# Optimization experiments

Measured on AMD Instinct MI355X. Metric: run time of the kernel, lower is better.

The kernel has to match this reference:

```python
import jax, jax.numpy as jnp
import numpy as np

B, S, D, H = 4, 2048, 512, 8

def setup_inputs() -> dict:
    key = jax.random.key(0)
    ks = jax.random.split(key, 6)
    query = jax.random.normal(ks[0], (B, S, D), dtype=jnp.float32)
    value = jax.random.normal(ks[1], (B, S, D), dtype=jnp.float32)
    # causal additive mask, broadcast over heads: [H, S, S]
    causal = jnp.where(jnp.tril(jnp.ones((S, S), dtype=bool)), 0.0, -1e9).astype(jnp.float32)
    mask = jnp.broadcast_to(causal[None, :, :], (H, S, S))
    sd = 1.0 / np.sqrt(D)
    Wq = jax.random.normal(ks[2], (D, D), dtype=jnp.float32) * sd
    Wkv = jax.random.normal(ks[3], (D, 2 * D), dtype=jnp.float32) * sd
    Wo = jax.random.normal(ks[4], (D, D), dtype=jnp.float32) * sd
    normalizer = jnp.asarray(1.0 / np.sqrt(D // H), dtype=jnp.float32)  # 1/sqrt(head_size)
    head_mults = jnp.ones((1, 1, H, 1), dtype=jnp.float32)
    return {"query": query, "value": value, "mask": mask, "Wq": Wq, "Wkv": Wkv,
            "Wo": Wo, "normalizer": normalizer, "head_mults": head_mults}

def reference(query, value, mask, Wq, Wkv, Wo, normalizer, head_mults):
    b, sq, d = query.shape
    h = head_mults.shape[2]
    q = (query @ Wq).reshape(b, sq, h, -1)                 # [b,q,h,hd]
    k, v = jnp.split(value @ Wkv, 2, axis=-1)
    sk = value.shape[1]
    k = k.reshape(b, sk, h, -1)
    v = v.reshape(b, sk, h, -1)
    score = jnp.einsum('bqhd,bkhd->bhqk', q, k) * normalizer
    score = score + mask[None, :, :, :]
    align = jax.nn.softmax(score, axis=-1)
    heads = jnp.einsum('bhqk,bkhd->bqhd', align, v)        # [b,q,h,hd]
    # cross-head normalization (over head axis, ddof=0 like tf.reduce_std)
    mean = jnp.mean(heads, axis=-2, keepdims=True)
    std = jnp.std(heads, axis=-2, keepdims=True)
    heads = (heads - mean) / (std + 0.01)
    heads = heads * head_mults
    out = heads.reshape(b, sq, d) @ Wo
    return out
```

## Files before the change

### kernel.cpp

```cpp
#include <hip/hip_runtime.h>


typedef float  f32x4  __attribute__((ext_vector_type(4)));
typedef __bf16 bf16x8 __attribute__((ext_vector_type(8)));
typedef short  s16x4  __attribute__((ext_vector_type(4)));
typedef unsigned short u16;

#define BS 2048
#define DD 512
#define NH 8
#define NQ (4 * BS * DD)

__device__ __forceinline__ u16 f2bf(float f) {
  union { float f; unsigned u; } v; v.f = f;
  unsigned r = v.u + 0x7fffu + ((v.u >> 16) & 1u);
  return (u16)(r >> 16);
}
__device__ __forceinline__ float bf2f(u16 b) {
  union { unsigned u; float f; } v; v.u = ((unsigned)b) << 16; return v.f;
}

__device__ __forceinline__ void gll16(const u16* g, u16* l) {
  __builtin_amdgcn_global_load_lds((const __attribute__((address_space(1))) void*)g,
                                   (__attribute__((address_space(3))) void*)l, 16, 0, 0);
}

__global__ __launch_bounds__(256) void prep(const float* __restrict__ q,
                                            const float* __restrict__ v,
                                            const float* __restrict__ Wq,
                                            const float* __restrict__ Wkv,
                                            const float* __restrict__ Wo,
                                            u16* __restrict__ qb, u16* __restrict__ vb,
                                            u16* __restrict__ WqT, u16* __restrict__ WkvT,
                                            u16* __restrict__ WoT) {
  __shared__ float Ts[64][65];
  const int t = threadIdx.x;
  int bx = blockIdx.x;
  if (bx < 8192) {
    int i = (bx * 256 + t) * 4;
    const float* s; u16* d;
    if (i < NQ) { s = q + i; d = qb + i; }
    else        { s = v + (i - NQ); d = vb + (i - NQ); }
    float4 x = *(const float4*)s;
    ushort4 o; o.x = f2bf(x.x); o.y = f2bf(x.y); o.z = f2bf(x.z); o.w = f2bf(x.w);
    *(ushort4*)d = o;
    return;
  }
  int tb = bx - 8192;
  const float* W; u16* Wt; int N, ntn;
  if (tb < 64)       { W = Wq;  Wt = WqT;  N = 512;  ntn = 8; }
  else if (tb < 192) { W = Wkv; Wt = WkvT; N = 1024; ntn = 16; tb -= 64; }
  else               { W = Wo;  Wt = WoT;  N = 512;  ntn = 8;  tb -= 192; }
  int tk = tb / ntn, tn = tb - tk * ntn;
  int r = t >> 2, c0 = (t & 3) * 16;
  const float* src = &W[(long)(tk * 64 + r) * N + tn * 64 + c0];
#pragma unroll
  for (int j = 0; j < 4; ++j) {
    float4 x = *(const float4*)(src + j * 4);
    Ts[r][c0 + j * 4 + 0] = x.x; Ts[r][c0 + j * 4 + 1] = x.y;
    Ts[r][c0 + j * 4 + 2] = x.z; Ts[r][c0 + j * 4 + 3] = x.w;
  }
  __syncthreads();
  u16* dst = &Wt[(long)(tn * 64 + r) * 512 + tk * 64 + c0];
#pragma unroll
  for (int m = 0; m < 4; ++m) {
    ushort4 o;
    o.x = f2bf(Ts[c0 + m * 4 + 0][r]); o.y = f2bf(Ts[c0 + m * 4 + 1][r]);
    o.z = f2bf(Ts[c0 + m * 4 + 2][r]); o.w = f2bf(Ts[c0 + m * 4 + 3][r]);
    *(ushort4*)(dst + m * 4) = o;
  }
}

__device__ __forceinline__ void gemm_core(const u16* __restrict__ A,
                                          const u16* __restrict__ Bt,
                                          int m0, int n0, int K,
                                          u16* Al, u16* Bl, f32x4 acc[4][4]) {
  const int t = threadIdx.x;
  const int wv = t >> 6, ln = t & 63, qd = ln >> 4, l16 = ln & 15;
  const int rw = (wv & 1) * 64, cw = (wv >> 1) * 64;
  const int sr = wv * 16 + (ln >> 2), sc = (ln & 3) * 8;
  for (int k0 = 0; k0 < K; k0 += 32) {
    __syncthreads();
#pragma unroll
    for (int c = 0; c < 2; ++c) {
      int r = c * 64 + sr;
      gll16(&A[(long)(m0 + r) * K + k0 + sc], &Al[r * 32 + sc]);
      gll16(&Bt[(long)(n0 + r) * K + k0 + sc], &Bl[r * 32 + sc]);
    }
    __syncthreads();
    bf16x8 af[4], bfr[4];
#pragma unroll
    for (int i = 0; i < 4; ++i) af[i] = *(const bf16x8*)&Al[(rw + i * 16 + l16) * 32 + qd * 8];
#pragma unroll
    for (int j = 0; j < 4; ++j) bfr[j] = *(const bf16x8*)&Bl[(cw + j * 16 + l16) * 32 + qd * 8];
#pragma unroll
    for (int i = 0; i < 4; ++i)
#pragma unroll
      for (int j = 0; j < 4; ++j)
        acc[i][j] = __builtin_amdgcn_mfma_f32_16x16x32_bf16(af[i], bfr[j], acc[i][j], 0, 0, 0);
  }
}

__global__ __launch_bounds__(256) void qkv_gemm(const u16* __restrict__ qA,
                                                const u16* __restrict__ vA,
                                                const u16* __restrict__ WqT,
                                                const u16* __restrict__ WkvT,
                                                u16* __restrict__ Qb,
                                                u16* __restrict__ Kb,
                                                u16* __restrict__ Vt) {
  __shared__ __align__(16) u16 Al[128 * 32];
  __shared__ __align__(16) u16 Bl[128 * 32];
  const bool isQ = blockIdx.y < 4;
  const u16* A = isQ ? qA : vA;
  const u16* Bt = isQ ? WqT : WkvT;
  const int n0 = (isQ ? blockIdx.y : blockIdx.y - 4) * 128;
  const int m0 = blockIdx.x * 128;
  f32x4 acc[4][4] = {};
  gemm_core(A, Bt, m0, n0, 512, Al, Bl, acc);
  const int t = threadIdx.x;
  const int wv = t >> 6, ln = t & 63, qd = ln >> 4, l16 = ln & 15;
  const int rw = (wv & 1) * 64, cw = (wv >> 1) * 64;
  if (isQ) {
#pragma unroll
    for (int i = 0; i < 4; ++i)
#pragma unroll
      for (int j = 0; j < 4; ++j) {
        int row = m0 + rw + i * 16 + qd * 4, col = n0 + cw + j * 16 + l16;
#pragma unroll
        for (int r = 0; r < 4; ++r)
          Qb[(long)(row + r) * 512 + col] = f2bf(acc[i][j][r]);
      }
  } else {
#pragma unroll
    for (int j = 0; j < 4; ++j) {
      int col = n0 + cw + j * 16 + l16;
      if (col < 512) {
#pragma unroll
        for (int i = 0; i < 4; ++i) {
          int row = m0 + rw + i * 16 + qd * 4;
#pragma unroll
          for (int r = 0; r < 4; ++r)
            Kb[(long)(row + r) * 512 + col] = f2bf(acc[i][j][r]);
        }
      } else {
        int c2 = col - 512, hh = c2 >> 6, dd = c2 & 63;
#pragma unroll
        for (int i = 0; i < 4; ++i) {
          int sg = m0 + rw + i * 16 + qd * 4;
          int bb = sg >> 11, ss = sg & 2047;
          ushort4 o;
          o.x = f2bf(acc[i][j][0]); o.y = f2bf(acc[i][j][1]);
          o.z = f2bf(acc[i][j][2]); o.w = f2bf(acc[i][j][3]);
          *(ushort4*)&Vt[((long)(bb * 8 + hh) * 64 + dd) * 2048 + ss] = o;
        }
      }
    }
  }
}

__global__ __launch_bounds__(256) void out_gemm(const u16* __restrict__ A,
                                                const u16* __restrict__ Bt,
                                                float* __restrict__ C) {
  __shared__ __align__(16) u16 Al[128 * 32];
  __shared__ __align__(16) u16 Bl[128 * 32];
  const int m0 = blockIdx.x * 128, n0 = blockIdx.y * 128;
  f32x4 acc[4][4] = {};
  gemm_core(A, Bt, m0, n0, 512, Al, Bl, acc);
  const int t = threadIdx.x;
  const int wv = t >> 6, ln = t & 63, qd = ln >> 4, l16 = ln & 15;
  const int rw = (wv & 1) * 64, cw = (wv >> 1) * 64;
#pragma unroll
  for (int i = 0; i < 4; ++i)
#pragma unroll
    for (int j = 0; j < 4; ++j) {
      int row = m0 + rw + i * 16 + qd * 4, col = n0 + cw + j * 16 + l16;
#pragma unroll
      for (int r = 0; r < 4; ++r)
        C[(long)(row + r) * 512 + col] = acc[i][j][r];
    }
}

__global__ __launch_bounds__(256, 4) void attn(const u16* __restrict__ Qb,
                                               const u16* __restrict__ Kb,
                                               const u16* __restrict__ Vt,
                                               u16* __restrict__ heads,
                                               const float* __restrict__ normp) {
  constexpr int ST = 72;
  __shared__ __align__(16) u16 Ks[2][64 * ST];
  __shared__ __align__(16) u16 Vts[2][64 * ST];
  const float scale2 = normp[0] * 1.44269504f;
  const int t = threadIdx.x;
  const int wv = t >> 6, ln = t & 63, qd = ln >> 4, l16 = ln & 15;
  const int sr = t >> 2, scg = (t & 3) * 16;
  const int h = blockIdx.y, b = blockIdx.z;
  const int bs0 = b * BS;
  const u16* vtb = Vt + ((long)(b * 8 + h) * 64) * 2048;

  for (int qsel = 0; qsel < 2; ++qsel) {
    const int qt = qsel ? (31 - (int)blockIdx.x) : (int)blockIdx.x;
    const int qi = qt * 64 + wv * 16 + l16;

    bf16x8 bq[2];
#pragma unroll
    for (int c = 0; c < 2; ++c)
      bq[c] = *(const bf16x8*)&Qb[(long)(bs0 + qi) * 512 + h * 64 + c * 32 + qd * 8];

    bf16x8 kr0, kr1, vr0, vr1;
#define FETCH(KB) do { \
      const u16* kp_ = &Kb[(long)(bs0 + (KB) * 64 + sr) * 512 + h * 64 + scg]; \
      kr0 = *(const bf16x8*)kp_; kr1 = *(const bf16x8*)(kp_ + 8); \
      const u16* vp_ = &vtb[(long)sr * 2048 + (KB) * 64 + scg]; \
      vr0 = *(const bf16x8*)vp_; vr1 = *(const bf16x8*)(vp_ + 8); } while (0)
    FETCH(0);
    float m_i = -1e30f, l_i = 0.f;
    f32x4 o[4] = {};

    for (int kb = 0; kb <= qt; ++kb) {
      const int buf = kb & 1;
      *(bf16x8*)&Ks[buf][sr * ST + scg] = kr0;
      *(bf16x8*)&Ks[buf][sr * ST + scg + 8] = kr1;
      *(bf16x8*)&Vts[buf][sr * ST + scg] = vr0;
      *(bf16x8*)&Vts[buf][sr * ST + scg + 8] = vr1;
      __syncthreads();
      if (kb < qt) FETCH(kb + 1);

      f32x4 s[4] = {};
#pragma unroll
      for (int c = 0; c < 2; ++c)
#pragma unroll
        for (int nt = 0; nt < 4; ++nt) {
          bf16x8 ak = *(const bf16x8*)&Ks[buf][(nt * 16 + l16) * ST + c * 32 + qd * 8];
          s[nt] = __builtin_amdgcn_mfma_f32_16x16x32_bf16(ak, bq[c], s[nt], 0, 0, 0);
        }

      const int limi = (kb == qt) ? (wv * 16 + l16) : 1 << 20;
      float mx = -1e30f;
#pragma unroll
      for (int nt = 0; nt < 4; ++nt)
#pragma unroll
        for (int r = 0; r < 4; ++r) {
          float v = s[nt][r] * scale2;
          if (nt * 16 + qd * 4 + r > limi) v = -1e30f;
          s[nt][r] = v;
          mx = fmaxf(mx, v);
        }
      mx = fmaxf(mx, __shfl_xor(mx, 16));
      mx = fmaxf(mx, __shfl_xor(mx, 32));
      float mn = fmaxf(m_i, mx);
      float al = exp2f(m_i - mn);
      float rs = 0.f;
#pragma unroll
      for (int nt = 0; nt < 4; ++nt)
#pragma unroll
        for (int r = 0; r < 4; ++r) {
          float p = exp2f(s[nt][r] - mn);
          s[nt][r] = p;
          rs += p;
        }
      rs += __shfl_xor(rs, 16);
      rs += __shfl_xor(rs, 32);
      l_i = l_i * al + rs;
      m_i = mn;
#pragma unroll
      for (int n2 = 0; n2 < 4; ++n2) o[n2] *= al;

#pragma unroll
      for (int cp = 0; cp < 2; ++cp) {
        bf16x8 pb;
        s16x4* ph = (s16x4*)&pb;
#pragma unroll
        for (int j = 0; j < 4; ++j) {
          ph[0][j] = (short)f2bf(s[cp * 2][j]);
          ph[1][j] = (short)f2bf(s[cp * 2 + 1][j]);
        }
#pragma unroll
        for (int n2 = 0; n2 < 4; ++n2) {
          bf16x8 av;
          s16x4* ah = (s16x4*)&av;
          const u16* vp = &Vts[buf][(n2 * 16 + l16) * ST + cp * 32 + qd * 4];
          ah[0] = *(const s16x4*)vp;
          ah[1] = *(const s16x4*)(vp + 16);
          o[n2] = __builtin_amdgcn_mfma_f32_16x16x32_bf16(av, pb, o[n2], 0, 0, 0);
        }
      }
    }
#undef FETCH

    float inv = 1.f / l_i;
    __syncthreads();
#pragma unroll
    for (int n2 = 0; n2 < 4; ++n2)
#pragma unroll
      for (int r = 0; r < 4; ++r)
        Ks[0][(wv * 16 + l16) * ST + n2 * 16 + qd * 4 + r] = f2bf(o[n2][r] * inv);
    __syncthreads();
    {
      u16* dst = &heads[(long)(bs0 + qt * 64 + sr) * 512 + h * 64 + scg];
      *(bf16x8*)dst = *(const bf16x8*)&Ks[0][sr * ST + scg];
      *(bf16x8*)(dst + 8) = *(const bf16x8*)&Ks[0][sr * ST + scg + 8];
    }
    __syncthreads();
  }
}

__global__ __launch_bounds__(256) void headnorm(const u16* __restrict__ heads,
                                                const float* __restrict__ hm,
                                                u16* __restrict__ outn) {
  int i = blockIdx.x * 256 + threadIdx.x;
  int d = i & 63, bs = i >> 6;
  const u16* p = heads + (long)bs * DD + d;
  float x[NH], mean = 0.f;
#pragma unroll
  for (int h = 0; h < NH; ++h) { x[h] = bf2f(p[h * 64]); mean += x[h]; }
  mean *= 0.125f;
  float var = 0.f;
#pragma unroll
  for (int h = 0; h < NH; ++h) { float dd = x[h] - mean; var += dd * dd; }
  var *= 0.125f;
  float inv = 1.f / (sqrtf(var) + 0.01f);
#pragma unroll
  for (int h = 0; h < NH; ++h)
    outn[(long)bs * DD + h * 64 + d] = f2bf((x[h] - mean) * inv * hm[h]);
}

extern "C" void kernel_launch(void* const* d_in, const int* in_sizes, int n_in,
                              void* d_out, int out_size, void* d_ws, size_t ws_size,
                              hipStream_t stream) {
  const float* query = (const float*)d_in[0];
  const float* value = (const float*)d_in[1];
  const float* Wq    = (const float*)d_in[3];
  const float* Wkv   = (const float*)d_in[4];
  const float* Wo    = (const float*)d_in[5];
  const float* normp = (const float*)d_in[6];
  const float* hmult = (const float*)d_in[7];

  char* ws = (char*)d_ws;
  const size_t MB = 1 << 20;
  u16*   qbf   = (u16*)(ws);
  u16*   vbf   = (u16*)(ws + 8 * MB);
  u16*   WqT   = (u16*)(ws + 16 * MB);
  u16*   WkvT  = (u16*)(ws + 16 * MB + 524288);
  u16*   WoT   = (u16*)(ws + 17 * MB + 524288);
  u16*   Qb    = (u16*)(ws + 18 * MB);
  u16*   Kb    = (u16*)(ws + 26 * MB);
  u16*   Vt    = (u16*)(ws + 34 * MB);
  u16*   heads = (u16*)(ws + 42 * MB);
  u16*   hN    = (u16*)(ws + 50 * MB);

  prep<<<8448, 256, 0, stream>>>(query, value, Wq, Wkv, Wo,
                                 qbf, vbf, WqT, WkvT, WoT);
  qkv_gemm<<<dim3(64, 12), 256, 0, stream>>>(qbf, vbf, WqT, WkvT, Qb, Kb, Vt);
  attn<<<dim3(16, NH, 4), 256, 0, stream>>>(Qb, Kb, Vt, heads, normp);
  headnorm<<<(4 * BS * 64) / 256, 256, 0, stream>>>(heads, hmult, hN);
  out_gemm<<<dim3(64, 4), 256, 0, stream>>>(hN, WoT, (float*)d_out);
}
```

Baseline: 293.9 us.

## Fuse fp32-to-bf16 activation conversion into QKV GEMM and widen K step

```diff
diff --git a/kernel.cpp b/kernel.cpp
--- a/kernel.cpp
+++ b/kernel.cpp
@@ -9,7 +9,6 @@
 #define BS 2048
 #define DD 512
 #define NH 8
-#define NQ (4 * BS * DD)
 
 __device__ __forceinline__ u16 f2bf(float f) {
   union { float f; unsigned u; } v; v.f = f;
@@ -19,34 +18,24 @@
 __device__ __forceinline__ float bf2f(u16 b) {
   union { unsigned u; float f; } v; v.u = ((unsigned)b) << 16; return v.f;
 }
+__device__ __forceinline__ u16 cvt1(float f) {
+  __bf16 h = (__bf16)f;
+  return __builtin_bit_cast(u16, h);
+}
 
 __device__ __forceinline__ void gll16(const u16* g, u16* l) {
   __builtin_amdgcn_global_load_lds((const __attribute__((address_space(1))) void*)g,
                                    (__attribute__((address_space(3))) void*)l, 16, 0, 0);
 }
 
-__global__ __launch_bounds__(256) void prep(const float* __restrict__ q,
-                                            const float* __restrict__ v,
-                                            const float* __restrict__ Wq,
+__global__ __launch_bounds__(256) void prep(const float* __restrict__ Wq,
                                             const float* __restrict__ Wkv,
                                             const float* __restrict__ Wo,
-                                            u16* __restrict__ qb, u16* __restrict__ vb,
                                             u16* __restrict__ WqT, u16* __restrict__ WkvT,
                                             u16* __restrict__ WoT) {
   __shared__ float Ts[64][65];
   const int t = threadIdx.x;
-  int bx = blockIdx.x;
-  if (bx < 8192) {
-    int i = (bx * 256 + t) * 4;
-    const float* s; u16* d;
-    if (i < NQ) { s = q + i; d = qb + i; }
-    else        { s = v + (i - NQ); d = vb + (i - NQ); }
-    float4 x = *(const float4*)s;
-    ushort4 o; o.x = f2bf(x.x); o.y = f2bf(x.y); o.z = f2bf(x.z); o.w = f2bf(x.w);
-    *(ushort4*)d = o;
-    return;
-  }
-  int tb = bx - 8192;
+  int tb = blockIdx.x;
   const float* W; u16* Wt; int N, ntn;
   if (tb < 64)       { W = Wq;  Wt = WqT;  N = 512;  ntn = 8; }
   else if (tb < 192) { W = Wkv; Wt = WkvT; N = 1024; ntn = 16; tb -= 64; }
@@ -71,52 +60,88 @@
   }
 }
 
-__device__ __forceinline__ void gemm_core(const u16* __restrict__ A,
-                                          const u16* __restrict__ Bt,
-                                          int m0, int n0, int K,
-                                          u16* Al, u16* Bl, f32x4 acc[4][4]) {
+template <int AF32>
+__device__ __forceinline__ void gemm_core64(const void* __restrict__ Av,
+                                            const u16* __restrict__ Bt,
+                                            int m0, int n0, int K,
+                                            u16* Al, u16* Bl, f32x4 acc[4][4]) {
   const int t = threadIdx.x;
   const int wv = t >> 6, ln = t & 63, qd = ln >> 4, l16 = ln & 15;
   const int rw = (wv & 1) * 64, cw = (wv >> 1) * 64;
-  const int sr = wv * 16 + (ln >> 2), sc = (ln & 3) * 8;
-  for (int k0 = 0; k0 < K; k0 += 32) {
-    __syncthreads();
-#pragma unroll
-    for (int c = 0; c < 2; ++c) {
-      int r = c * 64 + sr;
-      gll16(&A[(long)(m0 + r) * K + k0 + sc], &Al[r * 32 + sc]);
-      gll16(&Bt[(long)(n0 + r) * K + k0 + sc], &Bl[r * 32 + sc]);
-    }
-    __syncthreads();
-    bf16x8 af[4], bfr[4];
-#pragma unroll
-    for (int i = 0; i < 4; ++i) af[i] = *(const bf16x8*)&Al[(rw + i * 16 + l16) * 32 + qd * 8];
-#pragma unroll
-    for (int j = 0; j < 4; ++j) bfr[j] = *(const bf16x8*)&Bl[(cw + j * 16 + l16) * 32 + qd * 8];
-#pragma unroll
-    for (int i = 0; i < 4; ++i)
+  const int srB = wv * 16 + (ln >> 2), scB = (ln & 3) * 8;
+  const int srA = t >> 1, scA = (t & 1) * 16;
+  for (int k0 = 0; k0 < K; k0 += 64) {
+    __syncthreads();
+    if (AF32) {
+      const float* Af = (const float*)Av;
+#pragma unroll
+      for (int p = 0; p < 2; ++p) {
+        const float* src = &Af[(long)(m0 + srA) * K + k0 + p * 32 + scA];
+        float4 x0 = *(const float4*)src;
+        float4 x1 = *(const float4*)(src + 4);
+        float4 x2 = *(const float4*)(src + 8);
+        float4 x3 = *(const float4*)(src + 12);
+        bf16x8 o0, o1;
+        o0[0] = (__bf16)x0.x; o0[1] = (__bf16)x0.y; o0[2] = (__bf16)x0.z; o0[3] = (__bf16)x0.w;
+        o0[4] = (__bf16)x1.x; o0[5] = (__bf16)x1.y; o0[6] = (__bf16)x1.z; o0[7] = (__bf16)x1.w;
+        o1[0] = (__bf16)x2.x; o1[1] = (__bf16)x2.y; o1[2] = (__bf16)x2.z; o1[3] = (__bf16)x2.w;
+        o1[4] = (__bf16)x3.x; o1[5] = (__bf16)x3.y; o1[6] = (__bf16)x3.z; o1[7] = (__bf16)x3.w;
+        u16* dst = &Al[p * 4096 + srA * 32 + scA];
+        *(bf16x8*)dst = o0;
+        *(bf16x8*)(dst + 8) = o1;
+      }
+    } else {
+      const u16* Ab = (const u16*)Av;
+#pragma unroll
+      for (int p = 0; p < 2; ++p)
+#pragma unroll
+        for (int c = 0; c < 2; ++c) {
+          int r = c * 64 + srB;
+          gll16(&Ab[(long)(m0 + r) * K + k0 + p * 32 + scB], &Al[p * 4096 + r * 32 + scB]);
+        }
+    }
+#pragma unroll
+    for (int p = 0; p < 2; ++p)
+#pragma unroll
+      for (int c = 0; c < 2; ++c) {
+        int r = c * 64 + srB;
+        gll16(&Bt[(long)(n0 + r) * K + k0 + p * 32 + scB], &Bl[p * 4096 + r * 32 + scB]);
+      }
+    __syncthreads();
+#pragma unroll
+    for (int p = 0; p < 2; ++p) {
+      bf16x8 af[4], bfr[4];
+#pragma unroll
+      for (int i = 0; i < 4; ++i)
+        af[i] = *(const bf16x8*)&Al[p * 4096 + (rw + i * 16 + l16) * 32 + qd * 8];
 #pragma unroll
       for (int j = 0; j < 4; ++j)
-        acc[i][j] = __builtin_amdgcn_mfma_f32_16x16x32_bf16(af[i], bfr[j], acc[i][j], 0, 0, 0);
-  }
-}
-
-__global__ __launch_bounds__(256) void qkv_gemm(const u16* __restrict__ qA,
-                                                const u16* __restrict__ vA,
+        bfr[j] = *(const bf16x8*)&Bl[p * 4096 + (cw + j * 16 + l16) * 32 + qd * 8];
+#pragma unroll
+      for (int i = 0; i < 4; ++i)
+#pragma unroll
+        for (int j = 0; j < 4; ++j)
+          acc[i][j] = __builtin_amdgcn_mfma_f32_16x16x32_bf16(af[i], bfr[j], acc[i][j], 0, 0, 0);
+    }
+  }
+}
+
+__global__ __launch_bounds__(256) void qkv_gemm(const float* __restrict__ query,
+                                                const float* __restrict__ value,
                                                 const u16* __restrict__ WqT,
                                                 const u16* __restrict__ WkvT,
                                                 u16* __restrict__ Qb,
                                                 u16* __restrict__ Kb,
                                                 u16* __restrict__ Vt) {
-  __shared__ __align__(16) u16 Al[128 * 32];
-  __shared__ __align__(16) u16 Bl[128 * 32];
+  __shared__ __align__(16) u16 Al[2 * 128 * 32];
+  __shared__ __align__(16) u16 Bl[2 * 128 * 32];
   const bool isQ = blockIdx.y < 4;
-  const u16* A = isQ ? qA : vA;
+  const void* A = isQ ? (const void*)query : (const void*)value;
   const u16* Bt = isQ ? WqT : WkvT;
   const int n0 = (isQ ? blockIdx.y : blockIdx.y - 4) * 128;
   const int m0 = blockIdx.x * 128;
   f32x4 acc[4][4] = {};
-  gemm_core(A, Bt, m0, n0, 512, Al, Bl, acc);
+  gemm_core64<1>(A, Bt, m0, n0, 512, Al, Bl, acc);
   const int t = threadIdx.x;
   const int wv = t >> 6, ln = t & 63, qd = ln >> 4, l16 = ln & 15;
   const int rw = (wv & 1) * 64, cw = (wv >> 1) * 64;
@@ -128,7 +153,7 @@
         int row = m0 + rw + i * 16 + qd * 4, col = n0 + cw + j * 16 + l16;
 #pragma unroll
         for (int r = 0; r < 4; ++r)
-          Qb[(long)(row + r) * 512 + col] = f2bf(acc[i][j][r]);
+          Qb[(long)(row + r) * 512 + col] = cvt1(acc[i][j][r]);
       }
   } else {
 #pragma unroll
@@ -140,7 +165,7 @@
           int row = m0 + rw + i * 16 + qd * 4;
 #pragma unroll
           for (int r = 0; r < 4; ++r)
-            Kb[(long)(row + r) * 512 + col] = f2bf(acc[i][j][r]);
+            Kb[(long)(row + r) * 512 + col] = cvt1(acc[i][j][r]);
         }
       } else {
         int c2 = col - 512, hh = c2 >> 6, dd = c2 & 63;
@@ -149,8 +174,8 @@
           int sg = m0 + rw + i * 16 + qd * 4;
           int bb = sg >> 11, ss = sg & 2047;
           ushort4 o;
-          o.x = f2bf(acc[i][j][0]); o.y = f2bf(acc[i][j][1]);
-          o.z = f2bf(acc[i][j][2]); o.w = f2bf(acc[i][j][3]);
+          o.x = cvt1(acc[i][j][0]); o.y = cvt1(acc[i][j][1]);
+          o.z = cvt1(acc[i][j][2]); o.w = cvt1(acc[i][j][3]);
           *(ushort4*)&Vt[((long)(bb * 8 + hh) * 64 + dd) * 2048 + ss] = o;
         }
       }
@@ -161,11 +186,11 @@
 __global__ __launch_bounds__(256) void out_gemm(const u16* __restrict__ A,
                                                 const u16* __restrict__ Bt,
                                                 float* __restrict__ C) {
-  __shared__ __align__(16) u16 Al[128 * 32];
-  __shared__ __align__(16) u16 Bl[128 * 32];
+  __shared__ __align__(16) u16 Al[2 * 128 * 32];
+  __shared__ __align__(16) u16 Bl[2 * 128 * 32];
   const int m0 = blockIdx.x * 128, n0 = blockIdx.y * 128;
   f32x4 acc[4][4] = {};
-  gemm_core(A, Bt, m0, n0, 512, Al, Bl, acc);
+  gemm_core64<0>(A, Bt, m0, n0, 512, Al, Bl, acc);
   const int t = threadIdx.x;
   const int wv = t >> 6, ln = t & 63, qd = ln >> 4, l16 = ln & 15;
   const int rw = (wv & 1) * 64, cw = (wv >> 1) * 64;
@@ -267,11 +292,10 @@
 #pragma unroll
       for (int cp = 0; cp < 2; ++cp) {
         bf16x8 pb;
-        s16x4* ph = (s16x4*)&pb;
 #pragma unroll
         for (int j = 0; j < 4; ++j) {
-          ph[0][j] = (short)f2bf(s[cp * 2][j]);
-          ph[1][j] = (short)f2bf(s[cp * 2 + 1][j]);
+          pb[j] = (__bf16)s[cp * 2][j];
+          pb[4 + j] = (__bf16)s[cp * 2 + 1][j];
         }
 #pragma unroll
         for (int n2 = 0; n2 < 4; ++n2) {
@@ -292,7 +316,7 @@
     for (int n2 = 0; n2 < 4; ++n2)
 #pragma unroll
       for (int r = 0; r < 4; ++r)
-        Ks[0][(wv * 16 + l16) * ST + n2 * 16 + qd * 4 + r] = f2bf(o[n2][r] * inv);
+        Ks[0][(wv * 16 + l16) * ST + n2 * 16 + qd * 4 + r] = cvt1(o[n2][r] * inv);
     __syncthreads();
     {
       u16* dst = &heads[(long)(bs0 + qt * 64 + sr) * 512 + h * 64 + scg];
@@ -320,7 +344,7 @@
   float inv = 1.f / (sqrtf(var) + 0.01f);
 #pragma unroll
   for (int h = 0; h < NH; ++h)
-    outn[(long)bs * DD + h * 64 + d] = f2bf((x[h] - mean) * inv * hm[h]);
+    outn[(long)bs * DD + h * 64 + d] = cvt1((x[h] - mean) * inv * hm[h]);
 }
 
 extern "C" void kernel_launch(void* const* d_in, const int* in_sizes, int n_in,
@@ -336,20 +360,17 @@
 
   char* ws = (char*)d_ws;
   const size_t MB = 1 << 20;
-  u16*   qbf   = (u16*)(ws);
-  u16*   vbf   = (u16*)(ws + 8 * MB);
-  u16*   WqT   = (u16*)(ws + 16 * MB);
-  u16*   WkvT  = (u16*)(ws + 16 * MB + 524288);
-  u16*   WoT   = (u16*)(ws + 17 * MB + 524288);
-  u16*   Qb    = (u16*)(ws + 18 * MB);
-  u16*   Kb    = (u16*)(ws + 26 * MB);
-  u16*   Vt    = (u16*)(ws + 34 * MB);
-  u16*   heads = (u16*)(ws + 42 * MB);
-  u16*   hN    = (u16*)(ws + 50 * MB);
-
-  prep<<<8448, 256, 0, stream>>>(query, value, Wq, Wkv, Wo,
-                                 qbf, vbf, WqT, WkvT, WoT);
-  qkv_gemm<<<dim3(64, 12), 256, 0, stream>>>(qbf, vbf, WqT, WkvT, Qb, Kb, Vt);
+  u16*   WqT   = (u16*)(ws);
+  u16*   WkvT  = (u16*)(ws + 524288);
+  u16*   WoT   = (u16*)(ws + 1 * MB + 524288);
+  u16*   Qb    = (u16*)(ws + 2 * MB);
+  u16*   Kb    = (u16*)(ws + 10 * MB);
+  u16*   Vt    = (u16*)(ws + 18 * MB);
+  u16*   heads = (u16*)(ws + 26 * MB);
+  u16*   hN    = (u16*)(ws + 34 * MB);
+
+  prep<<<256, 256, 0, stream>>>(Wq, Wkv, Wo, WqT, WkvT, WoT);
+  qkv_gemm<<<dim3(64, 12), 256, 0, stream>>>(query, value, WqT, WkvT, Qb, Kb, Vt);
   attn<<<dim3(16, NH, 4), 256, 0, stream>>>(Qb, Kb, Vt, heads, normp);
   headnorm<<<(4 * BS * 64) / 256, 256, 0, stream>>>(heads, hmult, hN);
   out_gemm<<<dim3(64, 4), 256, 0, stream>>>(hN, WoT, (float*)d_out);
```

After: 287.2 us. 2.3% less time.
